# Kernel tuning notes

Measured on AMD Instinct MI355X. Metric: run time of the kernel, lower is better.

Reference implementation:

```python
import jax, jax.numpy as jnp
import numpy as np
from jax import lax

EPS = 1e-7
N_CLASS = 10
ROUTINGS = 3
DIM_PRIMARY = 8
DIM_DIGIT = 16


def squash(s, axis=-1):
    sq = jnp.sum(jnp.square(s), axis=axis, keepdims=True)
    scale = sq / (1.0 + sq) / jnp.sqrt(sq + EPS)
    return scale * s


def setup_inputs() -> dict:
    key = jax.random.key(0)
    ks = jax.random.split(key, 6)
    B, H, W, C = 16, 100, 64, 1
    x = jax.random.normal(ks[0], (B, H, W, C), dtype=jnp.float32)
    # conv1: 9x9, 1 -> 256, stride 1, valid, relu
    conv1_w = jax.random.normal(ks[1], (9, 9, 1, 256), dtype=jnp.float32) * 0.05
    conv1_b = jnp.zeros((256,), dtype=jnp.float32)
    # PrimaryCap conv: 9x9, 256 -> 32*8=256, stride 2, valid, linear
    pc_w = jax.random.normal(ks[2], (9, 9, 256, 256), dtype=jnp.float32) * 0.02
    pc_b = jnp.zeros((256,), dtype=jnp.float32)
    # primary caps: conv1 out 92x56 -> pc conv out 42x24 -> 42*24*32 = 32256 caps
    n_in_caps = 42 * 24 * 32
    caps_W = jax.random.normal(ks[3], (N_CLASS, n_in_caps, DIM_DIGIT, DIM_PRIMARY), dtype=jnp.float32) * 0.05
    return {"x": x, "conv1_w": conv1_w, "conv1_b": conv1_b, "pc_w": pc_w, "pc_b": pc_b, "caps_W": caps_W}


def reference(x, conv1_w, conv1_b, pc_w, pc_b, caps_W):
    dn = ("NHWC", "HWIO", "NHWC")
    # Conv1 + relu: [B,92,56,256]
    y = lax.conv_general_dilated(x, conv1_w, (1, 1), "VALID", dimension_numbers=dn) + conv1_b
    y = jax.nn.relu(y)
    # PrimaryCap conv (stride 2): [B,42,24,256]
    p = lax.conv_general_dilated(y, pc_w, (2, 2), "VALID", dimension_numbers=dn) + pc_b
    B = p.shape[0]
    # reshape to capsules [B, I, 8] and squash
    u = squash(p.reshape(B, -1, DIM_PRIMARY))
    # predictions u_hat[b,j,i,d] = W[j,i,d,k] u[b,i,k]  -> [B, J, I, 16]
    u_hat = jnp.einsum("bik,jidk->bjid", u, caps_W)
    # dynamic routing
    b = jnp.zeros(u_hat.shape[:3], dtype=u_hat.dtype)  # [B, J, I]
    v = None
    for r in range(ROUTINGS):
        c = jax.nn.softmax(b, axis=1)  # over output capsules J
        s = jnp.einsum("bji,bjid->bjd", c, u_hat)
        v = squash(s)  # [B, J, 16]
        if r < ROUTINGS - 1:
            b = b + jnp.einsum("bjd,bjid->bji", v, u_hat)
    return v
```

## Files before the change

kernel.cpp:

```cpp
#include <hip/hip_runtime.h>
#include <hip/hip_bf16.h>
#include <hip/hip_fp16.h>
#include <stdint.h>

typedef __bf16 bf16x8_t __attribute__((ext_vector_type(8)));
typedef float  f32x4_t  __attribute__((ext_vector_type(4)));

#define PLANE_H   (16L * 32256 * 32)
#define PSTRIDE_H 4128768L

__device__ __forceinline__ void gld_lds16(const void* g, void* l) {
    __builtin_amdgcn_global_load_lds(
        (const __attribute__((address_space(1))) uint32_t*)g,
        (__attribute__((address_space(3))) uint32_t*)l, 16, 0, 0);
}

__global__ __launch_bounds__(256) void k_conv1(
    const float* __restrict__ x, const float* __restrict__ w,
    const float* __restrict__ bias, __hip_bfloat16* __restrict__ y)
{
    const int b  = blockIdx.x / 92;
    const int oh = blockIdx.x % 92;
    const int oc = threadIdx.x;
    float wr[81];
#pragma unroll
    for (int t = 0; t < 81; ++t) wr[t] = w[t * 256 + oc];
    const float bs = bias[oc];
    const float* xb = x + (b * 100 + oh) * 64;
    __hip_bfloat16* yb = y + ((b * 92 + oh) * 56) * 256 + oc;
    for (int owg = 0; owg < 56; owg += 4) {
        float a0 = bs, a1 = bs, a2 = bs, a3 = bs;
#pragma unroll
        for (int kh = 0; kh < 9; ++kh) {
            const float* xr = xb + kh * 64 + owg;
            float xv[12];
#pragma unroll
            for (int t = 0; t < 12; ++t) xv[t] = xr[t];
#pragma unroll
            for (int kw = 0; kw < 9; ++kw) {
                const float wv = wr[kh * 9 + kw];
                a0 = fmaf(xv[kw + 0], wv, a0);
                a1 = fmaf(xv[kw + 1], wv, a1);
                a2 = fmaf(xv[kw + 2], wv, a2);
                a3 = fmaf(xv[kw + 3], wv, a3);
            }
        }
        yb[(owg + 0) * 256] = __float2bfloat16(fmaxf(a0, 0.f));
        yb[(owg + 1) * 256] = __float2bfloat16(fmaxf(a1, 0.f));
        yb[(owg + 2) * 256] = __float2bfloat16(fmaxf(a2, 0.f));
        yb[(owg + 3) * 256] = __float2bfloat16(fmaxf(a3, 0.f));
    }
}

__global__ __launch_bounds__(256) void k_wt(
    const float* __restrict__ w, __hip_bfloat16* __restrict__ wt)
{
    const int idx = blockIdx.x * 256 + threadIdx.x;
    const int oc  = idx / 20736;
    const int k   = idx - oc * 20736;
    wt[idx] = __float2bfloat16(w[k * 256 + oc]);
}

__global__ __launch_bounds__(256, 4) void k_pcconv3(
    const __hip_bfloat16* __restrict__ y,
    const __hip_bfloat16* __restrict__ wt,
    __half* __restrict__ pbase)
{
    __shared__ __hip_bfloat16 lA[128 * 64];
    __shared__ __hip_bfloat16 lB[128 * 64];
    const int gx  = blockIdx.x;
    const int nb  = gx & 1;
    const int tm  = gx >> 1;
    const int mbx = (tm & 7) * 16 + (tm >> 3);
    if (mbx >= 126) return;
    const int z = blockIdx.y;
    __half* __restrict__ p = pbase + (long)z * PSTRIDE_H;

    const int tid  = threadIdx.x;
    const int lane = tid & 63;
    const int w    = tid >> 6;
    const int oct  = lane >> 3;
    const int c    = (lane & 7) ^ oct;

    int ybaseA[4], wbB[4];
#pragma unroll
    for (int j = 0; j < 4; ++j) {
        const int r  = w * 32 + j * 8 + oct;
        const int m  = mbx * 128 + r;
        const int b  = m / 1008;
        const int rm = m - b * 1008;
        const int oh = rm / 24;
        const int ow = rm - oh * 24;
        ybaseA[j] = ((b * 92 + 2 * oh) * 56 + 2 * ow) * 256 + c * 8;
        wbB[j]    = (nb * 128 + r) * 20736 + c * 8;
    }

    f32x4_t acc[4][4];
#pragma unroll
    for (int mi = 0; mi < 4; ++mi)
#pragma unroll
        for (int ni = 0; ni < 4; ++ni)
            acc[mi][ni] = (f32x4_t){0.f, 0.f, 0.f, 0.f};

    const int mw = (w >> 1) * 64;
    const int nw = (w & 1) * 64;
    const int lr = lane & 15;
    const int lq = lane >> 4;
    const int koff0 = ((lq + 0) ^ (lr & 7)) * 8;
    const int koff1 = ((lq + 4) ^ (lr & 7)) * 8;

    const int off = (gx * 11 + z * 5) % 27;
    for (int it = 0; it < 27; ++it) {
        const int kc   = z * 27 + ((it + off) % 27);
        const int k0   = kc * 64;
        const int khw  = k0 >> 8;
        const int ic0  = k0 & 255;
        const int kh   = khw / 9;
        const int kw2  = khw - kh * 9;
        const int aoff = (kh * 56 + kw2) * 256 + ic0;
        __syncthreads();
#pragma unroll
        for (int j = 0; j < 4; ++j)
            gld_lds16(y + ybaseA[j] + aoff, &lA[(w * 32 + j * 8) * 64 + lane * 8]);
#pragma unroll
        for (int j = 0; j < 4; ++j)
            gld_lds16(wt + wbB[j] + k0, &lB[(w * 32 + j * 8) * 64 + lane * 8]);
        __builtin_amdgcn_s_waitcnt(0);
        __syncthreads();
#pragma unroll
        for (int t = 0; t < 2; ++t) {
            const int koff = t ? koff1 : koff0;
            bf16x8_t af[4], bfr[4];
#pragma unroll
            for (int mi = 0; mi < 4; ++mi)
                af[mi] = *(const bf16x8_t*)&lA[(mw + mi * 16 + lr) * 64 + koff];
#pragma unroll
            for (int ni = 0; ni < 4; ++ni)
                bfr[ni] = *(const bf16x8_t*)&lB[(nw + ni * 16 + lr) * 64 + koff];
#pragma unroll
            for (int mi = 0; mi < 4; ++mi)
#pragma unroll
                for (int ni = 0; ni < 4; ++ni)
                    acc[mi][ni] = __builtin_amdgcn_mfma_f32_16x16x32_bf16(
                        af[mi], bfr[ni], acc[mi][ni], 0, 0, 0);
        }
    }
#pragma unroll
    for (int mi = 0; mi < 4; ++mi)
#pragma unroll
        for (int ni = 0; ni < 4; ++ni) {
            const int col = nb * 128 + nw + ni * 16 + lr;
#pragma unroll
            for (int rr = 0; rr < 4; ++rr) {
                const int row = mbx * 128 + mw + mi * 16 + lq * 4 + rr;
                p[(long)row * 256 + col] = __float2half(acc[mi][ni][rr]);
            }
        }
}

__global__ __launch_bounds__(256) void k_squash(
    const __half* __restrict__ Ph, const float* __restrict__ bias, float* __restrict__ u)
{
    const int g = blockIdx.x * 256 + threadIdx.x;
    const long base = (long)g * 8;
    const int cb = (g & 31) * 8;
    float v[8];
#pragma unroll
    for (int t = 0; t < 8; ++t) v[t] = bias[cb + t];
#pragma unroll
    for (int z = 0; z < 12; ++z) {
        const uint4 r = *(const uint4*)(Ph + z * PSTRIDE_H + base);
        const unsigned wd[4] = {r.x, r.y, r.z, r.w};
#pragma unroll
        for (int h2 = 0; h2 < 4; ++h2) {
            const __half2 hh = *(const __half2*)&wd[h2];
            v[h2 * 2 + 0] += __low2float(hh);
            v[h2 * 2 + 1] += __high2float(hh);
        }
    }
    float sq = 0.f;
#pragma unroll
    for (int t = 0; t < 8; ++t) sq += v[t] * v[t];
    const float sc = sq / ((1.f + sq) * sqrtf(sq + 1e-7f));
#pragma unroll
    for (int t = 0; t < 8; ++t) u[base + t] = v[t] * sc;
}

__global__ __launch_bounds__(256) void k_uhat2(
    const float* __restrict__ u, const float* __restrict__ W, __half* __restrict__ uh,
    float* __restrict__ sp0)
{
    __shared__ __half lbuf[8 * 64 * 32];
    __shared__ float red[4 * 256];
    const int bh   = blockIdx.x;
    const int ic   = blockIdx.y;
    const int tid  = threadIdx.x;
    const int lane = tid & 63;
    const int wv   = tid >> 6;
    const int q    = tid & 3;
    const int il   = tid >> 2;
    const int i    = ic * 64 + il;

    for (int jg = 0; jg < 5; ++jg) {
        const float* wb0 = W + ((long)(2 * jg) * 32256 + i) * 128 + q * 32;
        const float* wb1 = wb0 + (long)32256 * 128;
        float4 w0[8], w1[8];
#pragma unroll
        for (int t = 0; t < 8; ++t) w0[t] = *(const float4*)(wb0 + t * 4);
#pragma unroll
        for (int t = 0; t < 8; ++t) w1[t] = *(const float4*)(wb1 + t * 4);
        if (jg) __syncthreads();
#pragma unroll
        for (int b = 0; b < 8; ++b) {
            const float* up = u + ((bh * 8 + b) * 32256 + i) * 8;
            const float4 u0 = *(const float4*)up;
            const float4 u1 = *(const float4*)(up + 4);
            union { __half h[8]; uint4 v; } pk;
#pragma unroll
            for (int d = 0; d < 4; ++d) {
                const float4 a = w0[2 * d], cc = w0[2 * d + 1];
                pk.h[d] = __float2half(
                    a.x * u0.x + a.y * u0.y + a.z * u0.z + a.w * u0.w +
                    cc.x * u1.x + cc.y * u1.y + cc.z * u1.z + cc.w * u1.w);
            }
#pragma unroll
            for (int d = 0; d < 4; ++d) {
                const float4 a = w1[2 * d], cc = w1[2 * d + 1];
                pk.h[4 + d] = __float2half(
                    a.x * u0.x + a.y * u0.y + a.z * u0.z + a.w * u0.w +
                    cc.x * u1.x + cc.y * u1.y + cc.z * u1.z + cc.w * u1.w);
            }
            *(uint4*)&lbuf[(b * 64 + il) * 32 + q * 8] = pk.v;
            float rv[8];
#pragma unroll
            for (int t = 0; t < 8; ++t) rv[t] = __half2float(pk.h[t]);
#pragma unroll
            for (int t = 0; t < 8; ++t) {
                rv[t] += __shfl_xor(rv[t], 4);
                rv[t] += __shfl_xor(rv[t], 8);
                rv[t] += __shfl_xor(rv[t], 16);
                rv[t] += __shfl_xor(rv[t], 32);
            }
            if (lane < 4) {
#pragma unroll
                for (int t = 0; t < 8; ++t)
                    red[wv * 256 + b * 32 + (t >> 2) * 16 + q * 4 + (t & 3)] = rv[t];
            }
        }
        __syncthreads();
        __half* pb = uh + (long)jg * PLANE_H + ((long)(bh * 8) * 32256 + ic * 64) * 32;
#pragma unroll
        for (int b = 0; b < 8; ++b) {
            const uint4 v = *(const uint4*)&lbuf[b * 2048 + tid * 8];
            *(uint4*)(pb + (long)b * (32256 * 32) + tid * 8) = v;
        }
        {
            const float v = red[tid] + red[256 + tid] + red[512 + tid] + red[768 + tid];
            const int bb = tid >> 5, j2 = (tid >> 4) & 1, dd = tid & 15;
            atomicAdd(&sp0[((bh * 8 + bb) * 10 + (2 * jg + j2)) * 16 + dd], 0.1f * v);
        }
    }
}

__global__ __launch_bounds__(256) void k_route4(
    const __half* __restrict__ uh, const float* __restrict__ vsum,
    float* __restrict__ sp)
{
    __shared__ float red[4 * 160];
    const int b     = blockIdx.x;
    const int chunk = blockIdx.y;
    const int tid   = threadIdx.x;
    const int lane  = tid & 63;
    const int wv    = tid >> 6;
    const int q     = lane & 3;
    const int ig    = lane >> 2;

    float vs[10][4];
#pragma unroll
    for (int j = 0; j < 10; ++j) {
        const float4 t = *(const float4*)(vsum + (b * 10 + j) * 16 + q * 4);
        vs[j][0] = t.x; vs[j][1] = t.y; vs[j][2] = t.z; vs[j][3] = t.w;
    }
    float acc[10][4];
#pragma unroll
    for (int j = 0; j < 10; ++j)
#pragma unroll
        for (int t = 0; t < 4; ++t) acc[j][t] = 0.f;

    const int ib = chunk * 576 + wv * 16 + ig;
    for (int ps = 0; ps < 9; ++ps) {
        const int i = ib + ps * 64;
        const long rb = ((long)b * 32256 + i) * 32 + q * 8;
        uint4 r[5];
#pragma unroll
        for (int jg = 0; jg < 5; ++jg)
            r[jg] = *(const uint4*)(uh + jg * PLANE_H + rb);
        float uhf[10][4];
#pragma unroll
        for (int jg = 0; jg < 5; ++jg) {
            const unsigned wd[4] = {r[jg].x, r[jg].y, r[jg].z, r[jg].w};
#pragma unroll
            for (int h2 = 0; h2 < 4; ++h2) {
                const __half2 hh = *(const __half2*)&wd[h2];
                const int j  = jg * 2 + (h2 >> 1);
                const int d0 = (h2 & 1) * 2;
                uhf[j][d0 + 0] = __low2float(hh);
                uhf[j][d0 + 1] = __high2float(hh);
            }
        }
        float logit[10];
#pragma unroll
        for (int j = 0; j < 10; ++j) {
            float lg = vs[j][0] * uhf[j][0] + vs[j][1] * uhf[j][1]
                     + vs[j][2] * uhf[j][2] + vs[j][3] * uhf[j][3];
            lg += __shfl_xor(lg, 1);
            lg += __shfl_xor(lg, 2);
            logit[j] = lg;
        }
        float mx = logit[0];
#pragma unroll
        for (int j = 1; j < 10; ++j) mx = fmaxf(mx, logit[j]);
        float den = 0.f, e[10];
#pragma unroll
        for (int j = 0; j < 10; ++j) { e[j] = __expf(logit[j] - mx); den += e[j]; }
        const float inv = __builtin_amdgcn_rcpf(den);
#pragma unroll
        for (int j = 0; j < 10; ++j) {
            const float c = e[j] * inv;
#pragma unroll
            for (int t = 0; t < 4; ++t) acc[j][t] = fmaf(c, uhf[j][t], acc[j][t]);
        }
    }
#pragma unroll
    for (int j = 0; j < 10; ++j)
#pragma unroll
        for (int t = 0; t < 4; ++t) {
            float v2 = acc[j][t];
            v2 += __shfl_xor(v2, 4);
            v2 += __shfl_xor(v2, 8);
            v2 += __shfl_xor(v2, 16);
            v2 += __shfl_xor(v2, 32);
            if (lane < 4) red[wv * 160 + j * 16 + q * 4 + t] = v2;
        }
    __syncthreads();
    if (tid < 160) {
        const float s = red[tid] + red[160 + tid] + red[320 + tid] + red[480 + tid];
        atomicAdd(&sp[b * 160 + tid], s);
    }
}

__global__ void k_finish(const float* __restrict__ sp, float* __restrict__ vsum,
                         float* __restrict__ out, const int fin)
{
    const int t = threadIdx.x;
    if (t >= 160) return;
    const float* s = sp + t * 16;
    float sv[16]; float sq = 0.f;
#pragma unroll
    for (int d = 0; d < 16; ++d) { sv[d] = s[d]; sq += sv[d] * sv[d]; }
    const float sc = sq / ((1.f + sq) * sqrtf(sq + 1e-7f));
    if (fin) {
#pragma unroll
        for (int d = 0; d < 16; ++d) out[t * 16 + d] = sv[d] * sc;
    } else {
        float* vp = vsum + t * 16;
#pragma unroll
        for (int d = 0; d < 16; ++d) vp[d] += sv[d] * sc;
    }
}

extern "C" void kernel_launch(void* const* d_in, const int* in_sizes, int n_in,
                              void* d_out, int out_size, void* d_ws, size_t ws_size,
                              hipStream_t stream)
{
    const float* x   = (const float*)d_in[0];
    const float* c1w = (const float*)d_in[1];
    const float* c1b = (const float*)d_in[2];
    const float* pcw = (const float*)d_in[3];
    const float* pcb = (const float*)d_in[4];
    const float* cW  = (const float*)d_in[5];
    float* out = (float*)d_out;

    char* ws = (char*)d_ws;
    float* u  = (float*)(ws);
    __half* Ph = (__half*)(ws + 16515072);
    __hip_bfloat16* y  = (__hip_bfloat16*)(ws + 115605504);
    __hip_bfloat16* wt = (__hip_bfloat16*)(ws + 157810688);
    __half* uh = (__half*)(ws + 16515072);
    float* sp   = (float*)(ws + 181665792);
    float* vsum = (float*)(ws + 181696512);

    hipMemsetAsync(sp, 0, (3 * 2560 + 2560) * 4, stream);

    k_conv1<<<16 * 92, 256, 0, stream>>>(x, c1w, c1b, y);
    k_wt<<<20736, 256, 0, stream>>>(pcw, wt);
    k_pcconv3<<<dim3(256, 12), 256, 0, stream>>>(y, wt, Ph);
    k_squash<<<2016, 256, 0, stream>>>(Ph, pcb, u);
    k_uhat2<<<dim3(2, 504), 256, 0, stream>>>(u, cW, uh, sp);
    k_finish<<<1, 256, 0, stream>>>(sp, vsum, out, 0);
    k_route4<<<dim3(16, 56), 256, 0, stream>>>(uh, vsum, sp + 2560);
    k_finish<<<1, 256, 0, stream>>>(sp + 2560, vsum, out, 0);
    k_route4<<<dim3(16, 56), 256, 0, stream>>>(uh, vsum, sp + 5120);
    k_finish<<<1, 256, 0, stream>>>(sp + 5120, vsum, out, 1);
}
```

Before: 709.9 us.

## Add 256x256-tile pipelined PrimaryCap conv GEMM with interleaved LDS loads and MFMA

Adds a new PrimaryCap conv kernel that uses 512 threads and a 256x256 output tile per block (63x12 grid) with 128KB of dynamic LDS, double buffered. Global-to-LDS loads for the next K step are split into quarters and interleaved with four MFMA phases, separated by barriers and s_setprio, so memory traffic overlaps compute. The larger tile raises data reuse and cuts the number of blocks. The cost is higher register and LDS pressure, a grid that may underfill the CUs, and a fallback path to the old kernel if the shared-memory attribute cannot be set.

```diff
diff --git a/kernel.cpp b/kernel.cpp
--- a/kernel.cpp
+++ b/kernel.cpp
@@ -158,6 +158,186 @@
         }
 }
 
+__global__ __launch_bounds__(512, 2) void k_pcconv8(
+    const __hip_bfloat16* __restrict__ y,
+    const __hip_bfloat16* __restrict__ wt,
+    __half* __restrict__ pbase)
+{
+    extern __shared__ __hip_bfloat16 sm[];
+    __hip_bfloat16* sA = sm;
+    __hip_bfloat16* sB = sm + 32768;
+
+    const int mblk = blockIdx.x;
+    const int z    = blockIdx.y;
+    __half* __restrict__ p = pbase + (long)z * PSTRIDE_H;
+
+    const int tid  = threadIdx.x;
+    const int lane = tid & 63;
+    const int w    = tid >> 6;
+    const int wm   = w >> 2;
+    const int wn   = w & 3;
+    const int oct  = lane >> 3;
+    const int c    = (lane & 7) ^ oct;
+
+    int ybs[4], wbs[4];
+#pragma unroll
+    for (int i64 = 0; i64 < 4; ++i64) {
+        const int r  = i64 * 64 + w * 8 + oct;
+        const int m  = mblk * 256 + r;
+        const int b  = m / 1008;
+        const int rm = m - b * 1008;
+        const int oh = rm / 24;
+        const int ow = rm - oh * 24;
+        ybs[i64] = ((b * 92 + 2 * oh) * 56 + 2 * ow) * 256 + c * 8;
+        wbs[i64] = r * 20736 + c * 8;
+    }
+    const int kbase = z * 1728;
+
+    auto aoffk = [&](int k0) {
+        const int khw = k0 >> 8;
+        const int kh  = khw / 9;
+        return (kh * 56 + (khw - kh * 9)) * 256 + (k0 & 255);
+    };
+    auto stA = [&](int i64, int buf, int aoff) {
+        gld_lds16(y + ybs[i64] + aoff, sA + buf * 16384 + (i64 * 64 + w * 8) * 64 + lane * 8);
+    };
+    auto stB = [&](int i64, int buf, int k0) {
+        gld_lds16(wt + wbs[i64] + k0, sB + buf * 16384 + (i64 * 64 + w * 8) * 64 + lane * 8);
+    };
+
+    f32x4_t acc[2][4][2][2];
+#pragma unroll
+    for (int mh = 0; mh < 2; ++mh)
+#pragma unroll
+        for (int mi = 0; mi < 4; ++mi)
+#pragma unroll
+            for (int nh = 0; nh < 2; ++nh)
+#pragma unroll
+                for (int ni = 0; ni < 2; ++ni)
+                    acc[mh][mi][nh][ni] = (f32x4_t){0.f, 0.f, 0.f, 0.f};
+
+    const int lr = lane & 15;
+    const int lq = lane >> 4;
+    const int koff0 = ((lq + 0) ^ (lr & 7)) * 8;
+    const int koff1 = ((lq + 4) ^ (lr & 7)) * 8;
+
+    bf16x8_t af[4][2], bf0[2][2], bf1[2][2];
+
+#define RD_A(CUR, MH)                                                                   \
+    _Pragma("unroll") for (int mi = 0; mi < 4; ++mi) {                                  \
+        const __hip_bfloat16* ap =                                                      \
+            sA + (CUR) * 16384 + (wm * 128 + (MH) * 64 + mi * 16 + lr) * 64;            \
+        af[mi][0] = *(const bf16x8_t*)(ap + koff0);                                     \
+        af[mi][1] = *(const bf16x8_t*)(ap + koff1);                                     \
+    }
+#define RD_B(DST, CUR, NH)                                                              \
+    _Pragma("unroll") for (int ni = 0; ni < 2; ++ni) {                                  \
+        const __hip_bfloat16* bp =                                                      \
+            sB + (CUR) * 16384 + (wn * 64 + (NH) * 32 + ni * 16 + lr) * 64;             \
+        DST[ni][0] = *(const bf16x8_t*)(bp + koff0);                                    \
+        DST[ni][1] = *(const bf16x8_t*)(bp + koff1);                                    \
+    }
+#define MFMA_Q(MH, NH, BF)                                                              \
+    _Pragma("unroll") for (int mi = 0; mi < 4; ++mi)                                    \
+    _Pragma("unroll") for (int ni = 0; ni < 2; ++ni) {                                  \
+        acc[MH][mi][NH][ni] = __builtin_amdgcn_mfma_f32_16x16x32_bf16(                  \
+            af[mi][0], BF[ni][0], acc[MH][mi][NH][ni], 0, 0, 0);                        \
+        acc[MH][mi][NH][ni] = __builtin_amdgcn_mfma_f32_16x16x32_bf16(                  \
+            af[mi][1], BF[ni][1], acc[MH][mi][NH][ni], 0, 0, 0);                        \
+    }
+
+    {
+        const int k0 = kbase;
+        const int ao = aoffk(k0);
+        stB(0, 0, k0); stB(1, 0, k0); stB(2, 0, k0); stB(3, 0, k0);
+        stA(0, 0, ao); stA(2, 0, ao); stA(1, 0, ao); stA(3, 0, ao);
+    }
+    asm volatile("s_waitcnt vmcnt(2)" ::: "memory");
+    __builtin_amdgcn_s_barrier();
+
+    for (int kt = 0; kt < 26; ++kt) {
+        const int cur = kt & 1, nxt = cur ^ 1;
+        const int k0n = kbase + (kt + 1) * 64;
+        const int aon = aoffk(k0n);
+        RD_A(cur, 0);
+        RD_B(bf0, cur, 0);
+        stB(0, nxt, k0n); stB(1, nxt, k0n);
+        __builtin_amdgcn_s_barrier();
+        asm volatile("s_waitcnt lgkmcnt(0)" ::: "memory");
+        __builtin_amdgcn_s_setprio(1);
+        MFMA_Q(0, 0, bf0);
+        __builtin_amdgcn_s_setprio(0);
+        __builtin_amdgcn_s_barrier();
+        RD_B(bf1, cur, 1);
+        stB(2, nxt, k0n); stB(3, nxt, k0n);
+        asm volatile("s_waitcnt vmcnt(4)" ::: "memory");
+        __builtin_amdgcn_s_barrier();
+        asm volatile("s_waitcnt lgkmcnt(0)" ::: "memory");
+        __builtin_amdgcn_s_setprio(1);
+        MFMA_Q(0, 1, bf1);
+        __builtin_amdgcn_s_setprio(0);
+        __builtin_amdgcn_s_barrier();
+        RD_A(cur, 1);
+        stA(0, nxt, aon); stA(2, nxt, aon);
+        __builtin_amdgcn_s_barrier();
+        asm volatile("s_waitcnt lgkmcnt(0)" ::: "memory");
+        __builtin_amdgcn_s_setprio(1);
+        MFMA_Q(1, 1, bf1);
+        __builtin_amdgcn_s_setprio(0);
+        __builtin_amdgcn_s_barrier();
+        stA(1, nxt, aon); stA(3, nxt, aon);
+        asm volatile("s_waitcnt vmcnt(2)" ::: "memory");
+        __builtin_amdgcn_s_barrier();
+        __builtin_amdgcn_s_setprio(1);
+        MFMA_Q(1, 0, bf0);
+        __builtin_amdgcn_s_setprio(0);
+        __builtin_amdgcn_s_barrier();
+    }
+
+    RD_A(0, 0);
+    RD_B(bf0, 0, 0);
+    __builtin_amdgcn_s_barrier();
+    asm volatile("s_waitcnt lgkmcnt(0)" ::: "memory");
+    __builtin_amdgcn_s_setprio(1);
+    MFMA_Q(0, 0, bf0);
+    __builtin_amdgcn_s_setprio(0);
+    __builtin_amdgcn_s_barrier();
+    RD_B(bf1, 0, 1);
+    asm volatile("s_waitcnt vmcnt(0)" ::: "memory");
+    __builtin_amdgcn_s_barrier();
+    asm volatile("s_waitcnt lgkmcnt(0)" ::: "memory");
+    __builtin_amdgcn_s_setprio(1);
+    MFMA_Q(0, 1, bf1);
+    __builtin_amdgcn_s_setprio(0);
+    __builtin_amdgcn_s_barrier();
+    RD_A(0, 1);
+    asm volatile("s_waitcnt lgkmcnt(0)" ::: "memory");
+    __builtin_amdgcn_s_setprio(1);
+    MFMA_Q(1, 1, bf1);
+    MFMA_Q(1, 0, bf0);
+    __builtin_amdgcn_s_setprio(0);
+
+#undef RD_A
+#undef RD_B
+#undef MFMA_Q
+
+#pragma unroll
+    for (int mh = 0; mh < 2; ++mh)
+#pragma unroll
+        for (int mi = 0; mi < 4; ++mi)
+#pragma unroll
+            for (int nh = 0; nh < 2; ++nh)
+#pragma unroll
+                for (int ni = 0; ni < 2; ++ni) {
+                    const int col = wn * 64 + nh * 32 + ni * 16 + lr;
+#pragma unroll
+                    for (int rr = 0; rr < 4; ++rr) {
+                        const int row = mblk * 256 + wm * 128 + mh * 64 + mi * 16 + lq * 4 + rr;
+                        p[(long)row * 256 + col] = __float2half(acc[mh][mi][nh][ni][rr]);
+                    }
+                }
+}
+
 __global__ __launch_bounds__(256) void k_squash(
     const __half* __restrict__ Ph, const float* __restrict__ bias, float* __restrict__ u)
 {
@@ -390,11 +570,20 @@
     float* sp   = (float*)(ws + 181665792);
     float* vsum = (float*)(ws + 181696512);
 
+    static int pc8_ok = -1;
+    if (pc8_ok < 0)
+        pc8_ok = (hipFuncSetAttribute((const void*)k_pcconv8,
+                    hipFuncAttributeMaxDynamicSharedMemorySize, 131072) == hipSuccess)
+                 ? 1 : 0;
+
     hipMemsetAsync(sp, 0, (3 * 2560 + 2560) * 4, stream);
 
     k_conv1<<<16 * 92, 256, 0, stream>>>(x, c1w, c1b, y);
     k_wt<<<20736, 256, 0, stream>>>(pcw, wt);
-    k_pcconv3<<<dim3(256, 12), 256, 0, stream>>>(y, wt, Ph);
+    if (pc8_ok)
+        k_pcconv8<<<dim3(63, 12), 512, 131072, stream>>>(y, wt, Ph);
+    else
+        k_pcconv3<<<dim3(256, 12), 256, 0, stream>>>(y, wt, Ph);
     k_squash<<<2016, 256, 0, stream>>>(Ph, pcb, u);
     k_uhat2<<<dim3(2, 504), 256, 0, stream>>>(u, cW, uh, sp);
     k_finish<<<1, 256, 0, stream>>>(sp, vsum, out, 0);
```

Result: faster. 650.7 us (-8.3%).
